# Kernel optimization log

Measured on AMD Instinct MI355X. Metric: run time of the kernel, lower is better.

The kernel has to match this reference:

```python
import jax, jax.numpy as jnp
import numpy as np

B, D_IN, D1, D2, D_PW, N_PW, N_DRUG = 8192, 19200, 512, 256, 128, 25, 1448


def setup_inputs() -> dict:
    key = jax.random.key(0)
    ks = jax.random.split(key, 11)
    s = 0.02  # param scale
    return {
        "x": jax.random.normal(ks[0], (B, D_IN), dtype=jnp.float32),
        "W1": jax.random.normal(ks[1], (D_IN, D1), dtype=jnp.float32) * s,
        "b1": jnp.zeros((D1,), jnp.float32),
        "W2": jax.random.normal(ks[2], (D1, D2), dtype=jnp.float32) * s,
        "b2": jnp.zeros((D2,), jnp.float32),
        "Wp": jax.random.normal(ks[3], (N_PW, D_PW, D2), dtype=jnp.float32) * s,
        "bp": jnp.zeros((N_PW, D_PW), jnp.float32),
        "Wd": jax.random.normal(ks[4], (N_DRUG, D_PW), dtype=jnp.float32) * s,
        "bd": jnp.zeros((N_DRUG,), jnp.float32),
        "drug_indices": jax.random.randint(ks[5], (B,), 0, N_DRUG, dtype=jnp.int32).astype(jnp.int64),
        "drug_pw": jax.random.randint(ks[6], (N_DRUG,), 0, N_PW, dtype=jnp.int32),
    }


def reference(x, W1, b1, W2, b2, Wp, bp, Wd, bd, drug_indices, drug_pw):
    # Shared encoder (eval mode: dropout is identity)
    h = jax.nn.relu(x @ W1 + b1)          # [B, 512]
    h = jax.nn.relu(h @ W2 + b2)          # [B, 256]
    # Pathway heads: compute all N_PW heads, then select per-sample pathway.
    pw_all = jax.nn.relu(jnp.einsum('bd,pkd->bpk', h, Wp) + bp)   # [B, P, 128]
    pw_idx = drug_pw[drug_indices]                                 # [B]
    pw_out = jnp.take_along_axis(pw_all, pw_idx[:, None, None], axis=1)[:, 0]  # [B, 128]
    # Per-drug linear head: gather each sample's drug weight row.
    w = Wd[drug_indices]                                           # [B, 128]
    return jnp.sum(pw_out * w, axis=-1) + bd[drug_indices]         # [B]
```

## Files before the change

### kernel.cpp

```cpp
#include <hip/hip_runtime.h>
#include <stdint.h>

#define B_SZ   8192
#define D_IN   19200
#define D1     512
#define D2     256
#define D_PW   128
#define N_PW   25

typedef __attribute__((ext_vector_type(8))) short bf16x8;
typedef __attribute__((ext_vector_type(4))) float f32x4;

#define DEV static __device__ __forceinline__

DEV unsigned short cvt1(float a) {
  unsigned int u = __builtin_bit_cast(unsigned int, a);
  u += 0x7FFFu + ((u >> 16) & 1u);
  return (unsigned short)(u >> 16);
}
DEV void load_lds16(const void* g, void* l) {
  __builtin_amdgcn_global_load_lds(
      (const __attribute__((address_space(1))) unsigned int*)g,
      (__attribute__((address_space(3))) unsigned int*)l, 16, 0, 0);
}

__global__ __launch_bounds__(256) void sort_kernel(
    const int* __restrict__ di_raw, const int* __restrict__ drug_pw,
    int* __restrict__ perm, int* __restrict__ dsamp, int* __restrict__ offs) {
  __shared__ int cnt[N_PW];
  __shared__ int off_s[N_PW + 1];
  __shared__ int anyodd;
  const int tid = threadIdx.x;
  if (tid < N_PW) cnt[tid] = 0;
  if (tid == 0) anyodd = 0;
  __syncthreads();
  int loc = 0;
  for (int i = tid; i < B_SZ / 2; i += 256) loc |= di_raw[2 * i + 1];
  if (loc) atomicOr(&anyodd, 1);
  __syncthreads();
  const int m64 = (anyodd == 0);
  for (int i = tid; i < B_SZ; i += 256) {
    int d = m64 ? di_raw[2 * i] : di_raw[i];
    dsamp[i] = d;
    atomicAdd(&cnt[drug_pw[d]], 1);
  }
  __syncthreads();
  if (tid == 0) {
    int s = 0;
    for (int p = 0; p < N_PW; p++) { off_s[p] = s; s += cnt[p]; }
    off_s[N_PW] = s;
    for (int p = 0; p <= N_PW; p++) offs[p] = off_s[p];
  }
  __syncthreads();
  if (tid < N_PW) cnt[tid] = off_s[tid];
  __syncthreads();
  for (int i = tid; i < B_SZ; i += 256) {
    int p = drug_pw[dsamp[i]];
    int pos = atomicAdd(&cnt[p], 1);
    perm[pos] = i;
  }
}

template <int NT>
__global__ __launch_bounds__(256) void transpose_cvt(
    const float* __restrict__ in, unsigned short* __restrict__ out, int R, int C) {
  __shared__ float tile[64][65];
  const int c0 = blockIdx.y * 64;
  const int t = threadIdx.x;
#pragma unroll 1
  for (int tt = 0; tt < NT; tt++) {
    int r0 = (blockIdx.x * NT + tt) * 64;
    float4 v[4];
#pragma unroll
    for (int rep = 0; rep < 4; rep++) {
      int idx = t + rep * 256;
      int row = idx >> 4, c4 = idx & 15;
      v[rep] = *(const float4*)(in + (size_t)(r0 + row) * C + c0 + c4 * 4);
    }
#pragma unroll
    for (int rep = 0; rep < 4; rep++) {
      int idx = t + rep * 256;
      int row = idx >> 4, c4 = idx & 15;
      tile[row][c4 * 4 + 0] = v[rep].x; tile[row][c4 * 4 + 1] = v[rep].y;
      tile[row][c4 * 4 + 2] = v[rep].z; tile[row][c4 * 4 + 3] = v[rep].w;
    }
    __syncthreads();
#pragma unroll
    for (int rep = 0; rep < 4; rep++) {
      int idx = t + rep * 256;
      int crow = idx >> 4, q = idx & 15;
      ushort4 o;
      o.x = cvt1(tile[q * 4 + 0][crow]);
      o.y = cvt1(tile[q * 4 + 1][crow]);
      o.z = cvt1(tile[q * 4 + 2][crow]);
      o.w = cvt1(tile[q * 4 + 3][crow]);
      *(ushort4*)(out + (size_t)(c0 + crow) * R + r0 + q * 4) = o;
    }
    __syncthreads();
  }
}

__global__ __launch_bounds__(256) void gemm1_kernel(
    const float* __restrict__ x, const unsigned short* __restrict__ w1t,
    const float* __restrict__ b1, unsigned short* __restrict__ h1) {
  __shared__ unsigned short As[64 * 32];
  __shared__ unsigned short Bs[128 * 32];
  const int t = threadIdx.x;
  const int lane = t & 63, wave = t >> 6;
  const int wm = wave & 1, wn = wave >> 1;
  const int l15 = lane & 15, l4 = lane >> 4;
  const int mb = blockIdx.x * 64, nb = blockIdx.y * 128;

  const float4* ag[2];
  ushort4* aw[2];
#pragma unroll
  for (int rep = 0; rep < 2; rep++) {
    int j = t + rep * 256;
    ag[rep] = (const float4*)(x + (size_t)(mb + (j >> 3)) * D_IN + (j & 7) * 4);
    aw[rep] = (ushort4*)(As + j * 4);
  }
  const unsigned short* bg[2];
  unsigned short* bl[2];
#pragma unroll
  for (int rep = 0; rep < 2; rep++) {
    int c = t + rep * 256;
    bg[rep] = w1t + (size_t)(nb + (c >> 2)) * D_IN + (c & 3) * 8;
    bl[rep] = Bs + ((t & ~63) + rep * 256) * 8;
  }
  const bf16x8* ar[2];
  const bf16x8* br[4];
#pragma unroll
  for (int i = 0; i < 2; i++)
    ar[i] = (const bf16x8*)(As + (wm * 32 + i * 16 + l15) * 32 + l4 * 8);
#pragma unroll
  for (int j = 0; j < 4; j++)
    br[j] = (const bf16x8*)(Bs + (wn * 64 + j * 16 + l15) * 32 + l4 * 8);

  f32x4 acc[2][4] = {};

  for (int kt = 0; kt < D_IN / 32; kt++) {
#pragma unroll
    for (int rep = 0; rep < 2; rep++) {
      float4 v = *ag[rep]; ag[rep] += 8;
      ushort4 o;
      o.x = cvt1(v.x); o.y = cvt1(v.y); o.z = cvt1(v.z); o.w = cvt1(v.w);
      *aw[rep] = o;
    }
#pragma unroll
    for (int rep = 0; rep < 2; rep++) {
      load_lds16(bg[rep], bl[rep]); bg[rep] += 32;
    }
    __syncthreads();
    bf16x8 a[2], b[4];
#pragma unroll
    for (int i = 0; i < 2; i++) a[i] = *ar[i];
#pragma unroll
    for (int j = 0; j < 4; j++) b[j] = *br[j];
#pragma unroll
    for (int i = 0; i < 2; i++)
#pragma unroll
      for (int j = 0; j < 4; j++)
        acc[i][j] = __builtin_amdgcn_mfma_f32_16x16x32_bf16(a[i], b[j], acc[i][j], 0, 0, 0);
    __syncthreads();
  }
#pragma unroll
  for (int j = 0; j < 4; j++) {
    int col = nb + wn * 64 + j * 16 + l15;
    float bias = b1[col];
#pragma unroll
    for (int i = 0; i < 2; i++) {
      int row0 = mb + wm * 32 + i * 16 + l4 * 4;
#pragma unroll
      for (int r = 0; r < 4; r++) {
        float v = acc[i][j][r] + bias;
        h1[(size_t)(row0 + r) * D1 + col] = cvt1(v > 0.f ? v : 0.f);
      }
    }
  }
}

__global__ __launch_bounds__(256) void gemm2_kernel(
    const unsigned short* __restrict__ h1, const unsigned short* __restrict__ w2t,
    const float* __restrict__ b2, unsigned short* __restrict__ h2) {
  __shared__ unsigned short As[128 * 32];
  __shared__ unsigned short Bs[128 * 32];
  const int t = threadIdx.x;
  const int lane = t & 63, wave = t >> 6;
  const int wm = wave & 1, wn = wave >> 1;
  const int l15 = lane & 15, l4 = lane >> 4;
  const int mb = blockIdx.x * 128, nb = blockIdx.y * 128;

  const unsigned short *ag[2], *bg[2];
  unsigned short *al[2], *bl[2];
#pragma unroll
  for (int rep = 0; rep < 2; rep++) {
    int c = t + rep * 256;
    ag[rep] = h1 + (size_t)(mb + (c >> 2)) * D1 + (c & 3) * 8;
    bg[rep] = w2t + (size_t)(nb + (c >> 2)) * D1 + (c & 3) * 8;
    al[rep] = As + ((t & ~63) + rep * 256) * 8;
    bl[rep] = Bs + ((t & ~63) + rep * 256) * 8;
  }
  const bf16x8* ar[4];
  const bf16x8* br[4];
#pragma unroll
  for (int i = 0; i < 4; i++) {
    ar[i] = (const bf16x8*)(As + (wm * 64 + i * 16 + l15) * 32 + l4 * 8);
    br[i] = (const bf16x8*)(Bs + (wn * 64 + i * 16 + l15) * 32 + l4 * 8);
  }
  f32x4 acc[4][4] = {};
  for (int kt = 0; kt < D1 / 32; kt++) {
#pragma unroll
    for (int rep = 0; rep < 2; rep++) {
      load_lds16(ag[rep], al[rep]); ag[rep] += 32;
      load_lds16(bg[rep], bl[rep]); bg[rep] += 32;
    }
    __syncthreads();
    bf16x8 a[4], b[4];
#pragma unroll
    for (int i = 0; i < 4; i++) a[i] = *ar[i];
#pragma unroll
    for (int j = 0; j < 4; j++) b[j] = *br[j];
#pragma unroll
    for (int i = 0; i < 4; i++)
#pragma unroll
      for (int j = 0; j < 4; j++)
        acc[i][j] = __builtin_amdgcn_mfma_f32_16x16x32_bf16(a[i], b[j], acc[i][j], 0, 0, 0);
    __syncthreads();
  }
#pragma unroll
  for (int j = 0; j < 4; j++) {
    int col = nb + wn * 64 + j * 16 + l15;
    float bias = b2[col];
#pragma unroll
    for (int i = 0; i < 4; i++) {
      int row0 = mb + wm * 64 + i * 16 + l4 * 4;
#pragma unroll
      for (int r = 0; r < 4; r++) {
        float v = acc[i][j][r] + bias;
        h2[(size_t)(row0 + r) * D2 + col] = cvt1(v > 0.f ? v : 0.f);
      }
    }
  }
}

__global__ __launch_bounds__(256) void pathway_kernel(
    const unsigned short* __restrict__ h2, const float* __restrict__ Wp,
    const float* __restrict__ bp, const float* __restrict__ Wd,
    const float* __restrict__ bd, const int* __restrict__ perm,
    const int* __restrict__ dsamp, const int* __restrict__ offs,
    float* __restrict__ out) {
  const int p = blockIdx.y;
  const int start = offs[p];
  const int cnt = offs[p + 1] - start;
  const int r0 = blockIdx.x * 128;
  if (r0 >= cnt) return;

  __shared__ unsigned short As[128 * 32];
  __shared__ unsigned short Bs[128 * 32];
  __shared__ int rowsmp[128];
  __shared__ int dl[128];
  __shared__ float rowacc[128];

  const int t = threadIdx.x;
  const int lane = t & 63, wave = t >> 6;
  const int wm = wave & 1, wn = wave >> 1;
  const int l15 = lane & 15, l4 = lane >> 4;

  if (t < 128) {
    int r = r0 + t;
    int s = perm[start + (r < cnt ? r : 0)];
    rowsmp[t] = s;
    dl[t] = dsamp[s];
    rowacc[t] = 0.f;
  }
  __syncthreads();

  const unsigned short* ag[2];
  unsigned short* al[2];
#pragma unroll
  for (int rep = 0; rep < 2; rep++) {
    int c = t + rep * 256;
    ag[rep] = h2 + (size_t)rowsmp[c >> 2] * D2 + (c & 3) * 8;
    al[rep] = As + ((t & ~63) + rep * 256) * 8;
  }
  const float4* bg[4];
  ushort4* bw[4];
#pragma unroll
  for (int rep = 0; rep < 4; rep++) {
    int j = t + rep * 256;
    bg[rep] = (const float4*)(Wp + ((size_t)p * D_PW + (j >> 3)) * D2 + (j & 7) * 4);
    bw[rep] = (ushort4*)(Bs + j * 4);
  }
  const bf16x8* ar[4];
  const bf16x8* br[4];
#pragma unroll
  for (int i = 0; i < 4; i++) {
    ar[i] = (const bf16x8*)(As + (wm * 64 + i * 16 + l15) * 32 + l4 * 8);
    br[i] = (const bf16x8*)(Bs + (wn * 64 + i * 16 + l15) * 32 + l4 * 8);
  }

  f32x4 acc[4][4] = {};
  for (int kt = 0; kt < D2 / 32; kt++) {
#pragma unroll
    for (int rep = 0; rep < 2; rep++) {
      load_lds16(ag[rep], al[rep]); ag[rep] += 32;
    }
#pragma unroll
    for (int rep = 0; rep < 4; rep++) {
      float4 v = *bg[rep]; bg[rep] += 8;
      ushort4 o;
      o.x = cvt1(v.x); o.y = cvt1(v.y); o.z = cvt1(v.z); o.w = cvt1(v.w);
      *bw[rep] = o;
    }
    __syncthreads();
    bf16x8 a[4], b[4];
#pragma unroll
    for (int i = 0; i < 4; i++) a[i] = *ar[i];
#pragma unroll
    for (int j = 0; j < 4; j++) b[j] = *br[j];
#pragma unroll
    for (int i = 0; i < 4; i++)
#pragma unroll
      for (int j = 0; j < 4; j++)
        acc[i][j] = __builtin_amdgcn_mfma_f32_16x16x32_bf16(a[i], b[j], acc[i][j], 0, 0, 0);
    __syncthreads();
  }

  float p16[4][4];
#pragma unroll
  for (int i = 0; i < 4; i++)
#pragma unroll
    for (int r = 0; r < 4; r++) p16[i][r] = 0.f;

#pragma unroll
  for (int j = 0; j < 4; j++) {
    int col = wn * 64 + j * 16 + l15;
    float bias = bp[p * D_PW + col];
#pragma unroll
    for (int i = 0; i < 4; i++) {
      int rowl0 = wm * 64 + i * 16 + l4 * 4;
#pragma unroll
      for (int r = 0; r < 4; r++) {
        float v = acc[i][j][r] + bias;
        v = v > 0.f ? v : 0.f;
        p16[i][r] += v * Wd[(size_t)dl[rowl0 + r] * D_PW + col];
      }
    }
  }
#pragma unroll
  for (int off = 1; off < 16; off <<= 1) {
#pragma unroll
    for (int i = 0; i < 4; i++)
#pragma unroll
      for (int r = 0; r < 4; r++)
        p16[i][r] += __shfl_xor(p16[i][r], off, 16);
  }
  if (l15 == 0) {
#pragma unroll
    for (int i = 0; i < 4; i++)
#pragma unroll
      for (int r = 0; r < 4; r++)
        atomicAdd(&rowacc[wm * 64 + i * 16 + l4 * 4 + r], p16[i][r]);
  }
  __syncthreads();
  if (t < 128 && r0 + t < cnt) {
    out[rowsmp[t]] = rowacc[t] + bd[dl[t]];
  }
}

extern "C" void kernel_launch(void* const* d_in, const int* in_sizes, int n_in,
                              void* d_out, int out_size, void* d_ws, size_t ws_size,
                              hipStream_t stream) {
  const float* x       = (const float*)d_in[0];
  const float* W1      = (const float*)d_in[1];
  const float* b1      = (const float*)d_in[2];
  const float* W2      = (const float*)d_in[3];
  const float* b2      = (const float*)d_in[4];
  const float* Wp      = (const float*)d_in[5];
  const float* bp      = (const float*)d_in[6];
  const float* Wd      = (const float*)d_in[7];
  const float* bd      = (const float*)d_in[8];
  const int*   di_raw  = (const int*)d_in[9];
  const int*   drug_pw = (const int*)d_in[10];
  float* out = (float*)d_out;

  char* ws = (char*)d_ws;
  size_t o = 0;
  unsigned short* W1T = (unsigned short*)(ws + o); o += (size_t)D1 * D_IN * 2;
  unsigned short* W2T = (unsigned short*)(ws + o); o += (size_t)D2 * D1 * 2;
  unsigned short* h1  = (unsigned short*)(ws + o); o += (size_t)B_SZ * D1 * 2;
  unsigned short* h2  = (unsigned short*)(ws + o); o += (size_t)B_SZ * D2 * 2;
  int* perm  = (int*)(ws + o); o += (size_t)B_SZ * 4;
  int* dsamp = (int*)(ws + o); o += (size_t)B_SZ * 4;
  int* offs  = (int*)(ws + o); o += 128;
  (void)in_sizes; (void)n_in; (void)out_size; (void)ws_size;

  sort_kernel<<<1, 256, 0, stream>>>(di_raw, drug_pw, perm, dsamp, offs);
  transpose_cvt<4><<<dim3(D_IN / 256, D1 / 64), 256, 0, stream>>>(W1, W1T, D_IN, D1);
  transpose_cvt<1><<<dim3(D1 / 64, D2 / 64), 256, 0, stream>>>(W2, W2T, D1, D2);
  gemm1_kernel<<<dim3(B_SZ / 64, D1 / 128), 256, 0, stream>>>(x, W1T, b1, h1);
  gemm2_kernel<<<dim3(B_SZ / 128, D2 / 128), 256, 0, stream>>>(h1, W2T, b2, h2);
  pathway_kernel<<<dim3(64, N_PW), 256, 0, stream>>>(h2, Wp, bp, Wd, bd,
                                                     perm, dsamp, offs, out);
}
```

Baseline: 1.355 ms.

## Double-buffer gemm1 LDS tiles with register prefetch and swizzled layout

Rewrites the gemm1 main loop as a software pipeline. The W1 tile for the next step goes into a second LDS buffer via direct global-to-LDS loads, and the fp32 x tile two steps ahead is prefetched into registers, then converted and stored while the current tile feeds MFMA. This leaves one barrier per iteration instead of two. It also XOR-swizzles the LDS layout of both A and B to reduce bank conflicts on the bf16x8 reads. The change depends on hand-placed waitcnt and sched_barrier calls and doubles LDS use per block, which may lower occupancy.

```diff
diff --git a/kernel.cpp b/kernel.cpp
--- a/kernel.cpp
+++ b/kernel.cpp
@@ -103,66 +103,104 @@
 __global__ __launch_bounds__(256) void gemm1_kernel(
     const float* __restrict__ x, const unsigned short* __restrict__ w1t,
     const float* __restrict__ b1, unsigned short* __restrict__ h1) {
-  __shared__ unsigned short As[64 * 32];
-  __shared__ unsigned short Bs[128 * 32];
+  __shared__ unsigned short As[2][64 * 32];
+  __shared__ unsigned short Bs[2][128 * 32];
   const int t = threadIdx.x;
   const int lane = t & 63, wave = t >> 6;
   const int wm = wave & 1, wn = wave >> 1;
   const int l15 = lane & 15, l4 = lane >> 4;
   const int mb = blockIdx.x * 64, nb = blockIdx.y * 128;
-
-  const float4* ag[2];
-  ushort4* aw[2];
+  constexpr int NKT = D_IN / 32;
+
+  const float* ab[2];
+  int aw_off[2];
 #pragma unroll
   for (int rep = 0; rep < 2; rep++) {
     int j = t + rep * 256;
-    ag[rep] = (const float4*)(x + (size_t)(mb + (j >> 3)) * D_IN + (j & 7) * 4);
-    aw[rep] = (ushort4*)(As + j * 4);
-  }
-  const unsigned short* bg[2];
-  unsigned short* bl[2];
+    int row = j >> 3, c4 = j & 7;
+    ab[rep] = x + (size_t)(mb + row) * D_IN + c4 * 4;
+    int slot = (c4 >> 1) ^ ((row >> 1) & 3);
+    aw_off[rep] = row * 32 + slot * 8 + (c4 & 1) * 4;
+  }
+  const unsigned short* bgb[2];
+  unsigned short* bld[2][2];
 #pragma unroll
   for (int rep = 0; rep < 2; rep++) {
     int c = t + rep * 256;
-    bg[rep] = w1t + (size_t)(nb + (c >> 2)) * D_IN + (c & 3) * 8;
-    bl[rep] = Bs + ((t & ~63) + rep * 256) * 8;
-  }
-  const bf16x8* ar[2];
-  const bf16x8* br[4];
+    int row = c >> 2, s = c & 3;
+    int sg = s ^ ((row >> 1) & 3);
+    bgb[rep] = w1t + (size_t)(nb + row) * D_IN + sg * 8;
+    int dst = ((t & ~63) + rep * 256) * 8;
+    bld[0][rep] = &Bs[0][dst];
+    bld[1][rep] = &Bs[1][dst];
+  }
+  const int swz = (l15 >> 1) & 3;
+  int ar_off[2], br_off[4];
 #pragma unroll
   for (int i = 0; i < 2; i++)
-    ar[i] = (const bf16x8*)(As + (wm * 32 + i * 16 + l15) * 32 + l4 * 8);
+    ar_off[i] = (wm * 32 + i * 16 + l15) * 32 + (l4 ^ swz) * 8;
 #pragma unroll
   for (int j = 0; j < 4; j++)
-    br[j] = (const bf16x8*)(Bs + (wn * 64 + j * 16 + l15) * 32 + l4 * 8);
+    br_off[j] = (wn * 64 + j * 16 + l15) * 32 + (l4 ^ swz) * 8;
 
   f32x4 acc[2][4] = {};
-
-  for (int kt = 0; kt < D_IN / 32; kt++) {
-#pragma unroll
-    for (int rep = 0; rep < 2; rep++) {
-      float4 v = *ag[rep]; ag[rep] += 8;
-      ushort4 o;
-      o.x = cvt1(v.x); o.y = cvt1(v.y); o.z = cvt1(v.z); o.w = cvt1(v.w);
-      *aw[rep] = o;
-    }
-#pragma unroll
-    for (int rep = 0; rep < 2; rep++) {
-      load_lds16(bg[rep], bl[rep]); bg[rep] += 32;
-    }
-    __syncthreads();
-    bf16x8 a[2], b[4];
-#pragma unroll
-    for (int i = 0; i < 2; i++) a[i] = *ar[i];
-#pragma unroll
-    for (int j = 0; j < 4; j++) b[j] = *br[j];
-#pragma unroll
-    for (int i = 0; i < 2; i++)
-#pragma unroll
-      for (int j = 0; j < 4; j++)
-        acc[i][j] = __builtin_amdgcn_mfma_f32_16x16x32_bf16(a[i], b[j], acc[i][j], 0, 0, 0);
-    __syncthreads();
-  }
+  float4 areg0[2], areg1[2];
+
+#pragma unroll
+  for (int rep = 0; rep < 2; rep++) load_lds16(bgb[rep], bld[0][rep]);
+  __builtin_amdgcn_sched_barrier(0);
+#pragma unroll
+  for (int rep = 0; rep < 2; rep++) areg0[rep] = *(const float4*)(ab[rep]);
+#pragma unroll
+  for (int rep = 0; rep < 2; rep++) areg1[rep] = *(const float4*)(ab[rep] + 32);
+  __builtin_amdgcn_sched_barrier(0);
+#pragma unroll
+  for (int rep = 0; rep < 2; rep++) {
+    ushort4 o;
+    o.x = cvt1(areg0[rep].x); o.y = cvt1(areg0[rep].y);
+    o.z = cvt1(areg0[rep].z); o.w = cvt1(areg0[rep].w);
+    *(ushort4*)(&As[0][aw_off[rep]]) = o;
+  }
+  asm volatile("s_waitcnt lgkmcnt(0)" ::: "memory");
+  __builtin_amdgcn_s_barrier();
+  __builtin_amdgcn_sched_barrier(0);
+
+#define G1_BODY(KT, P0, P1, APRE, ACVT)                                        \
+  {                                                                            \
+    const int kb = ((KT) + 1 < NKT) ? (KT) + 1 : NKT - 1;                      \
+    const int ka = ((KT) + 2 < NKT) ? (KT) + 2 : NKT - 1;                      \
+    _Pragma("unroll") for (int rep = 0; rep < 2; rep++)                        \
+        load_lds16(bgb[rep] + (size_t)kb * 32, bld[P1][rep]);                  \
+    __builtin_amdgcn_sched_barrier(0);                                         \
+    _Pragma("unroll") for (int rep = 0; rep < 2; rep++)                        \
+        APRE[rep] = *(const float4*)(ab[rep] + (size_t)ka * 32);               \
+    __builtin_amdgcn_sched_barrier(0);                                         \
+    _Pragma("unroll") for (int rep = 0; rep < 2; rep++) {                      \
+      ushort4 o;                                                               \
+      o.x = cvt1(ACVT[rep].x); o.y = cvt1(ACVT[rep].y);                        \
+      o.z = cvt1(ACVT[rep].z); o.w = cvt1(ACVT[rep].w);                        \
+      *(ushort4*)(&As[P1][aw_off[rep]]) = o;                                   \
+    }                                                                          \
+    bf16x8 a[2], b[4];                                                         \
+    _Pragma("unroll") for (int i = 0; i < 2; i++)                              \
+        a[i] = *(const bf16x8*)(&As[P0][ar_off[i]]);                           \
+    _Pragma("unroll") for (int j = 0; j < 4; j++)                              \
+        b[j] = *(const bf16x8*)(&Bs[P0][br_off[j]]);                           \
+    _Pragma("unroll") for (int i = 0; i < 2; i++)                              \
+        _Pragma("unroll") for (int j = 0; j < 4; j++)                          \
+            acc[i][j] = __builtin_amdgcn_mfma_f32_16x16x32_bf16(               \
+                a[i], b[j], acc[i][j], 0, 0, 0);                               \
+    asm volatile("s_waitcnt vmcnt(2) lgkmcnt(0)" ::: "memory");                \
+    __builtin_amdgcn_s_barrier();                                              \
+    __builtin_amdgcn_sched_barrier(0);                                         \
+  }
+
+  for (int kt = 0; kt < NKT; kt += 2) {
+    G1_BODY(kt, 0, 1, areg0, areg1)
+    G1_BODY(kt + 1, 1, 0, areg1, areg0)
+  }
+#undef G1_BODY
+
 #pragma unroll
   for (int j = 0; j < 4; j++) {
     int col = nb + wn * 64 + j * 16 + l15;
```

Measured after the change: 1.225 ms. -9.5%, faster.
